# Kernel tuning notes

Measured on AMD Instinct MI355X. Metric: run time of the kernel, lower is better.

Reference implementation:

```python
import jax, jax.numpy as jnp
import numpy as np

KERNEL = 7  # neighborhood window (7x7)
NUM_HEADS = 4


def _window_idx(L, k):
    # NATTEN edge-clamped window start: each query attends to exactly k neighbors.
    starts = jnp.clip(jnp.arange(L) - k // 2, 0, L - k)  # [L]
    return starts[:, None] + jnp.arange(k)[None, :]       # [L, k]


def setup_inputs() -> dict:
    key = jax.random.key(0)
    k1, k2, k3, k4, k5 = jax.random.split(key, 5)
    B, H, W, D = 8, 64, 64, 128
    return {
        "x": jax.random.normal(k1, (B, H, W, D), dtype=jnp.float32),
        "w_qkv": jax.random.normal(k2, (3 * D, D), dtype=jnp.float32) * 0.02,
        "b_qkv": jax.random.normal(k3, (3 * D,), dtype=jnp.float32) * 0.02,
        "w_proj": jax.random.normal(k4, (D, D), dtype=jnp.float32) * 0.02,
        "b_proj": jax.random.normal(k5, (D,), dtype=jnp.float32) * 0.02,
    }


def reference(x, w_qkv, b_qkv, w_proj, b_proj):
    B, H, W, D = x.shape
    nh, k = NUM_HEADS, KERNEL
    hd = D // nh
    scale = hd ** -0.5

    # QKV projection -> [3, B, nh, H, W, hd]
    qkv = x @ w_qkv.T + b_qkv
    qkv = qkv.reshape(B, H, W, 3, nh, hd).transpose(3, 0, 4, 1, 2, 5)
    q, kk, v = qkv[0], qkv[1], qkv[2]

    idx_h = _window_idx(H, k)  # [H, k]
    idx_w = _window_idx(W, k)  # [W, k]
    IH = idx_h[:, None, :, None]  # [H,1,k,1]
    IW = idx_w[None, :, None, :]  # [1,W,1,k]

    # Gather local K/V neighborhoods: [B, nh, H, W, k, k, hd] -> [B, nh, H, W, k*k, hd]
    kn = kk[:, :, IH, IW, :].reshape(B, nh, H, W, k * k, hd)
    vn = v[:, :, IH, IW, :].reshape(B, nh, H, W, k * k, hd)

    attn = jnp.einsum('bhxyd,bhxynd->bhxyn', q * scale, kn)
    attn = jax.nn.softmax(attn, axis=-1)
    out = jnp.einsum('bhxyn,bhxynd->bhxyd', attn, vn)

    out = out.transpose(0, 2, 3, 1, 4).reshape(B, H, W, D)
    return out @ w_proj.T + b_proj
```

## Files before the change

### kernel.cpp

```cpp
#include <hip/hip_runtime.h>
#include <hip/hip_bf16.h>

#define BB 8
#define HH 64
#define WW 64
#define DD 128
#define NH 4
#define HD 32
#define KS 7
#define TS 8
#define HALO 14

typedef __attribute__((ext_vector_type(8))) short short8v;
typedef __attribute__((ext_vector_type(4))) short short4v;
typedef __attribute__((ext_vector_type(4))) float f32x4;
typedef unsigned short bf16_t;

__device__ inline bf16_t f2bf(float f) {
  __hip_bfloat16 h = __float2bfloat16(f);
  return *reinterpret_cast<bf16_t*>(&h);
}

__global__ __launch_bounds__(256) void qkv_mfma(
    const float* __restrict__ x, const float* __restrict__ w,
    const float* __restrict__ bqkv,
    bf16_t* __restrict__ q, bf16_t* __restrict__ k, bf16_t* __restrict__ v) {
  __shared__ __align__(16) short smA[128 * 128];
  __shared__ __align__(16) short smB[128 * 128];
  const int tid = threadIdx.x;
  const int m_tile = blockIdx.x;
  const int n_tile = blockIdx.y;

  const float* Ab = x + (size_t)m_tile * 128 * 128;
  const float* Bb = w + (size_t)n_tile * 128 * 128;
#pragma unroll
  for (int i = 0; i < 8; i++) {
    int idx = tid + i * 256;
    int r = idx >> 4, p = idx & 15;
    const float* ap = Ab + r * 128 + p * 8;
    float4 a0 = *(const float4*)ap;
    float4 a1 = *(const float4*)(ap + 4);
    short8v s;
    s[0] = f2bf(a0.x); s[1] = f2bf(a0.y); s[2] = f2bf(a0.z); s[3] = f2bf(a0.w);
    s[4] = f2bf(a1.x); s[5] = f2bf(a1.y); s[6] = f2bf(a1.z); s[7] = f2bf(a1.w);
    *(short8v*)((char*)smA + ((r * 256 + p * 16) ^ ((r & 7) << 4))) = s;
    const float* bp_ = Bb + r * 128 + p * 8;
    float4 b0 = *(const float4*)bp_;
    float4 b1 = *(const float4*)(bp_ + 4);
    short8v t;
    t[0] = f2bf(b0.x); t[1] = f2bf(b0.y); t[2] = f2bf(b0.z); t[3] = f2bf(b0.w);
    t[4] = f2bf(b1.x); t[5] = f2bf(b1.y); t[6] = f2bf(b1.z); t[7] = f2bf(b1.w);
    *(short8v*)((char*)smB + ((r * 256 + p * 16) ^ ((r & 7) << 4))) = t;
  }
  __syncthreads();

  const int lane = tid & 63;
  const int wid = tid >> 6;
  const int wm = wid >> 1, wn = wid & 1;
  const int l15 = lane & 15, l4 = lane >> 4;

  f32x4 acc[4][4] = {};
  const int rowA0 = wm * 64 + l15;
  const int rowB0 = wn * 64 + l15;
  const int swzA = (rowA0 & 7) << 4;
  const int swzB = (rowB0 & 7) << 4;

#pragma unroll
  for (int ks = 0; ks < 4; ks++) {
    const int cb = ks * 64 + l4 * 16;
    short8v a[4], b[4];
#pragma unroll
    for (int i = 0; i < 4; i++) {
      a[i] = *(const short8v*)((const char*)smA + ((((rowA0 + i * 16) * 256) + cb) ^ swzA));
      b[i] = *(const short8v*)((const char*)smB + ((((rowB0 + i * 16) * 256) + cb) ^ swzB));
    }
#pragma unroll
    for (int mi = 0; mi < 4; mi++)
#pragma unroll
      for (int nj = 0; nj < 4; nj++)
        acc[mi][nj] = __builtin_amdgcn_mfma_f32_16x16x32_bf16(a[mi], b[nj], acc[mi][nj], 0, 0, 0);
  }

  __syncthreads();
  short* smC = smA;
  const float qscale = 0.17677669529663687f;
#pragma unroll
  for (int nj = 0; nj < 4; nj++) {
    const int n_local = wn * 64 + nj * 16 + l15;
    const int n = n_tile * 128 + n_local;
    const float bias = bqkv[n];
    const float sc = (n_tile == 0) ? qscale : 1.f;
#pragma unroll
    for (int mi = 0; mi < 4; mi++) {
#pragma unroll
      for (int r = 0; r < 4; r++) {
        const int m = wm * 64 + mi * 16 + l4 * 4 + r;
        *(bf16_t*)((char*)smC + ((m * 256 + n_local * 2) ^ ((m & 7) << 4))) =
            (bf16_t)f2bf((acc[mi][nj][r] + bias) * sc);
      }
    }
  }
  __syncthreads();

  const int bblk = m_tile >> 5;
  bf16_t* outp = (n_tile == 0) ? q : ((n_tile == 1) ? k : v);
#pragma unroll
  for (int i = 0; i < 8; i++) {
    const int idx = i * 256 + tid;
    const int h = idx >> 9;
    const int rem = idx & 511;
    const int m = rem >> 2, c = rem & 3;
    short8v t8 = *(const short8v*)((const char*)smC +
        ((m * 256 + h * 64 + c * 16) ^ ((m & 7) << 4)));
    const int pix = (m_tile * 128 + m) & 4095;
    *(short8v*)(outp + ((size_t)(bblk * 4 + h)) * 131072 + (size_t)pix * 32 + c * 8) = t8;
  }
}

__global__ __launch_bounds__(256) void attn_mfma(
    const bf16_t* __restrict__ q, const bf16_t* __restrict__ k,
    const bf16_t* __restrict__ v, bf16_t* __restrict__ ao) {
  __shared__ __align__(16) char vtb[16384];

  const int tile = blockIdx.x;
  const int tx = tile >> 3, ty = tile & 7;
  const int head = blockIdx.y, bb = blockIdx.z;
  const size_t bh = ((size_t)bb * NH + head) * 4096;
  const bf16_t* kb = k + bh * HD;
  const bf16_t* vb = v + bh * HD;
  const bf16_t* qb = q + bh * HD;
  const int rstart = min(max(tx * TS - 3, 0), HH - HALO);
  const int cstart = min(max(ty * TS - 3, 0), WW - HALO);
  const int tid = threadIdx.x;
  const int lane = tid & 63, wid = tid >> 6;
  const int l15 = lane & 15, h4 = lane >> 4;

  short8v qf;
  int qx, qy;
  {
    const int pit = wid * 16 + l15;
    qx = tx * TS + (pit >> 3);
    qy = ty * TS + (pit & 7);
    qf = *(const short8v*)(qb + ((size_t)(qx * WW + qy)) * HD + h4 * 8);
  }
  const int wx0 = min(max(qx - 3, 0), HH - KS) - rstart;
  const int wy0 = min(max(qy - 3, 0), WW - KS) - cstart;

  const int x0 = tx * TS + wid * 2;
  const int w0 = min(max(x0 - 3, 0), HH - KS) - rstart;
  const int base = min(w0 & ~1, 4);

  short4v vl[4][2];
#pragma unroll
  for (int t = 0; t < 4; t++) {
    const int idx = tid + t * 256;
    if (idx < 784) {
      const int pp = idx >> 3, c = idx & 7;
      const int pr = pp / 7, pc2 = (pp % 7) * 2;
      const size_t g = ((size_t)((rstart + pr) * WW + (cstart + pc2))) * HD + c * 4;
      vl[t][0] = *(const short4v*)(vb + g);
      vl[t][1] = *(const short4v*)(vb + g + HD);
    }
  }

  f32x4 acc[10];
  const f32x4 zf = {0.f, 0.f, 0.f, 0.f};
  const int kcol = cstart + min(l15, 13);
#pragma unroll
  for (int ch = 0; ch < 2; ch++) {
    short8v kf[5];
#pragma unroll
    for (int i = 0; i < 5; i++) {
      const int pr = rstart + base + ch * 5 + i;
      kf[i] = *(const short8v*)(kb + ((size_t)(pr * WW + kcol)) * HD + h4 * 8);
    }
    __builtin_amdgcn_s_setprio(1);
#pragma unroll
    for (int i = 0; i < 5; i++)
      acc[ch * 5 + i] = __builtin_amdgcn_mfma_f32_16x16x32_bf16(kf[i], qf, zf, 0, 0, 0);
    __builtin_amdgcn_s_setprio(0);
  }

#pragma unroll
  for (int t = 0; t < 4; t++) {
    const int idx = tid + t * 256;
    if (idx < 784) {
      const int pp = idx >> 3, c = idx & 7;
      const int pr = pp / 7, pc2 = (pp % 7) * 2;
      const int pos0 = ((pr >> 1) << 5) + ((pc2 >> 2) << 3) + ((pr & 1) << 2) + (pc2 & 3);
#pragma unroll
      for (int j = 0; j < 4; j++) {
        const int d = c * 4 + j;
        const unsigned pk2 = (unsigned)(unsigned short)vl[t][0][j] |
                             ((unsigned)(unsigned short)vl[t][1][j] << 16);
        *(unsigned*)(vtb + ((d * 512 + pos0 * 2) ^ ((d & 7) << 4))) = pk2;
      }
    }
  }
  for (int idx = tid; idx < 512; idx += 256) {
    const int d = idx >> 4, pr = idx & 15;
    if (pr < 14) {
      const int pos = ((pr >> 1) << 5) + 24 + ((pr & 1) << 2) + 2;
      *(unsigned*)(vtb + ((d * 512 + pos * 2) ^ ((d & 7) << 4))) = 0u;
    }
  }
  __syncthreads();

  bool cv[4];
#pragma unroll
  for (int r = 0; r < 4; r++) cv[r] = ((unsigned)(h4 * 4 + r - wy0) < 7u);
  float sum = 0.f;
#pragma unroll
  for (int nt = 0; nt < 10; nt++) {
    const bool rv = ((unsigned)(base + nt - wx0) < 7u);
#pragma unroll
    for (int r = 0; r < 4; r++) {
      const float p = (rv && cv[r]) ? __expf(acc[nt][r]) : 0.f;
      acc[nt][r] = p;
      sum += p;
    }
  }
  sum += __shfl_xor(sum, 16);
  sum += __shfl_xor(sum, 32);
  const float inv = 1.f / sum;

  f32x4 o0 = zf, o1 = zf;
  const int swzv = (l15 & 7) << 4;
  const int cbase = (base >> 1) * 64;
  __builtin_amdgcn_s_setprio(1);
#pragma unroll
  for (int kc = 0; kc < 5; kc++) {
    union { unsigned u[4]; short8v s; } pa;
    pa.u[0] = (unsigned)f2bf(acc[2 * kc][0] * inv) |
              ((unsigned)f2bf(acc[2 * kc][1] * inv) << 16);
    pa.u[1] = (unsigned)f2bf(acc[2 * kc][2] * inv) |
              ((unsigned)f2bf(acc[2 * kc][3] * inv) << 16);
    pa.u[2] = (unsigned)f2bf(acc[2 * kc + 1][0] * inv) |
              ((unsigned)f2bf(acc[2 * kc + 1][1] * inv) << 16);
    pa.u[3] = (unsigned)f2bf(acc[2 * kc + 1][2] * inv) |
              ((unsigned)f2bf(acc[2 * kc + 1][3] * inv) << 16);
    const int boff = cbase + kc * 64 + h4 * 16;
    short8v vb0 = *(const short8v*)(vtb + ((l15 * 512 + boff) ^ swzv));
    short8v vb1 = *(const short8v*)(vtb + (((l15 + 16) * 512 + boff) ^ swzv));
    o0 = __builtin_amdgcn_mfma_f32_16x16x32_bf16(pa.s, vb0, o0, 0, 0, 0);
    o1 = __builtin_amdgcn_mfma_f32_16x16x32_bf16(pa.s, vb1, o1, 0, 0, 0);
  }
  __builtin_amdgcn_s_setprio(0);

#pragma unroll
  for (int r = 0; r < 4; r++) {
    const int pit = wid * 16 + h4 * 4 + r;
    const int x = tx * TS + (pit >> 3), y = ty * TS + (pit & 7);
    bf16_t* op = ao + ((size_t)bb * 4096 + x * WW + y) * DD + head * HD;
    op[l15]      = (bf16_t)f2bf(o0[r]);
    op[l15 + 16] = (bf16_t)f2bf(o1[r]);
  }
}

__global__ __launch_bounds__(256) void proj_mfma(
    const bf16_t* __restrict__ aob, const float* __restrict__ wp,
    const float* __restrict__ bp, float* __restrict__ out) {
  __shared__ __align__(16) char plds[65536];
  short* smA = (short*)plds;
  short* smB = (short*)(plds + 32768);
  const int tid = threadIdx.x;
  const int m_tile = blockIdx.x;

  const bf16_t* Ab = aob + (size_t)m_tile * 128 * 128;
#pragma unroll
  for (int i = 0; i < 8; i++) {
    int idx = tid + i * 256;
    int r = idx >> 4, p = idx & 15;
    short8v s = *(const short8v*)(Ab + r * 128 + p * 8);
    *(short8v*)((char*)smA + ((r * 256 + p * 16) ^ ((r & 7) << 4))) = s;
    const float* bp_ = wp + r * 128 + p * 8;
    float4 b0 = *(const float4*)bp_;
    float4 b1 = *(const float4*)(bp_ + 4);
    short8v t;
    t[0] = f2bf(b0.x); t[1] = f2bf(b0.y); t[2] = f2bf(b0.z); t[3] = f2bf(b0.w);
    t[4] = f2bf(b1.x); t[5] = f2bf(b1.y); t[6] = f2bf(b1.z); t[7] = f2bf(b1.w);
    *(short8v*)((char*)smB + ((r * 256 + p * 16) ^ ((r & 7) << 4))) = t;
  }
  __syncthreads();

  const int lane = tid & 63;
  const int wid = tid >> 6;
  const int wm = wid >> 1, wn = wid & 1;
  const int l15 = lane & 15, l4 = lane >> 4;

  f32x4 acc[4][4] = {};
  const int rowA0 = wm * 64 + l15;
  const int rowB0 = wn * 64 + l15;
  const int swzA = (rowA0 & 7) << 4;
  const int swzB = (rowB0 & 7) << 4;

#pragma unroll
  for (int ks = 0; ks < 4; ks++) {
    const int cb = ks * 64 + l4 * 16;
    short8v a[4], b[4];
#pragma unroll
    for (int i = 0; i < 4; i++) {
      a[i] = *(const short8v*)((const char*)smA + ((((rowA0 + i * 16) * 256) + cb) ^ swzA));
      b[i] = *(const short8v*)((const char*)smB + ((((rowB0 + i * 16) * 256) + cb) ^ swzB));
    }
#pragma unroll
    for (int mi = 0; mi < 4; mi++)
#pragma unroll
      for (int nj = 0; nj < 4; nj++)
        acc[mi][nj] = __builtin_amdgcn_mfma_f32_16x16x32_bf16(a[mi], b[nj], acc[mi][nj], 0, 0, 0);
  }

  __syncthreads();
#pragma unroll
  for (int nj = 0; nj < 4; nj++) {
    const int n = wn * 64 + nj * 16 + l15;
    const float bias = bp[n];
#pragma unroll
    for (int mi = 0; mi < 4; mi++) {
#pragma unroll
      for (int r = 0; r < 4; r++) {
        const int m = wm * 64 + mi * 16 + l4 * 4 + r;
        *(float*)(plds + ((m * 512 + n * 4) ^ ((m & 7) << 5))) = acc[mi][nj][r] + bias;
      }
    }
  }
  __syncthreads();

#pragma unroll
  for (int i = 0; i < 16; i++) {
    const int idx = i * 256 + tid;
    const int m = idx >> 5, c = idx & 31;
    float4 t = *(const float4*)(plds + ((m * 512 + c * 16) ^ ((m & 7) << 5)));
    *(float4*)(out + (size_t)(m_tile * 128 + m) * DD + c * 4) = t;
  }
}

extern "C" void kernel_launch(void* const* d_in, const int* in_sizes, int n_in,
                              void* d_out, int out_size, void* d_ws, size_t ws_size,
                              hipStream_t stream) {
  const float* x      = (const float*)d_in[0];
  const float* w_qkv  = (const float*)d_in[1];
  const float* b_qkv  = (const float*)d_in[2];
  const float* w_proj = (const float*)d_in[3];
  const float* b_proj = (const float*)d_in[4];
  float* out = (float*)d_out;

  const size_t per = (size_t)BB * NH * HH * WW * HD;
  bf16_t* q  = (bf16_t*)d_ws;
  bf16_t* k  = q + per;
  bf16_t* v  = k + per;
  bf16_t* ao = v + per;

  qkv_mfma<<<dim3(256, 3), dim3(256), 0, stream>>>(x, w_qkv, b_qkv, q, k, v);
  attn_mfma<<<dim3(64, NH, BB), dim3(256), 0, stream>>>(q, k, v, ao);
  proj_mfma<<<dim3(256), dim3(256), 0, stream>>>(ao, w_proj, b_proj, out);
}
```

Measured before the change: 43.74 us.

## Pre-convert weights to bf16 and shrink GEMM tiles, reading B from global

Adds a small kernel that converts the QKV and projection weights to bf16 once per call, so the GEMM kernels no longer convert fp32 weights per block. The QKV GEMM tile shrinks from 128 to 64 rows and the projection tile from 128 to 32 rows, which raises the block count and cuts LDS use. Weight fragments are now loaded straight from global memory instead of being staged in LDS. In exchange there is an extra kernel launch and more redundant weight reads across blocks, served from cache.

```diff
diff --git a/kernel.cpp b/kernel.cpp
--- a/kernel.cpp
+++ b/kernel.cpp
@@ -21,20 +21,34 @@
   return *reinterpret_cast<bf16_t*>(&h);
 }
 
+__global__ __launch_bounds__(256) void convert_w(
+    const float* __restrict__ wq, const float* __restrict__ wp,
+    bf16_t* __restrict__ wqb, bf16_t* __restrict__ wpb) {
+  const int chunk = blockIdx.x * 256 + threadIdx.x;
+  if (chunk < 12288) {
+    float4 t = *(const float4*)(wq + chunk * 4);
+    short4v s = {(short)f2bf(t.x), (short)f2bf(t.y), (short)f2bf(t.z), (short)f2bf(t.w)};
+    *(short4v*)(wqb + chunk * 4) = s;
+  } else {
+    const int c2 = chunk - 12288;
+    float4 t = *(const float4*)(wp + c2 * 4);
+    short4v s = {(short)f2bf(t.x), (short)f2bf(t.y), (short)f2bf(t.z), (short)f2bf(t.w)};
+    *(short4v*)(wpb + c2 * 4) = s;
+  }
+}
+
 __global__ __launch_bounds__(256) void qkv_mfma(
-    const float* __restrict__ x, const float* __restrict__ w,
+    const float* __restrict__ x, const bf16_t* __restrict__ wqb,
     const float* __restrict__ bqkv,
     bf16_t* __restrict__ q, bf16_t* __restrict__ k, bf16_t* __restrict__ v) {
-  __shared__ __align__(16) short smA[128 * 128];
-  __shared__ __align__(16) short smB[128 * 128];
+  __shared__ __align__(16) short smA[64 * 128];
   const int tid = threadIdx.x;
   const int m_tile = blockIdx.x;
   const int n_tile = blockIdx.y;
 
-  const float* Ab = x + (size_t)m_tile * 128 * 128;
-  const float* Bb = w + (size_t)n_tile * 128 * 128;
-#pragma unroll
-  for (int i = 0; i < 8; i++) {
+  const float* Ab = x + (size_t)m_tile * 64 * 128;
+#pragma unroll
+  for (int i = 0; i < 4; i++) {
     int idx = tid + i * 256;
     int r = idx >> 4, p = idx & 15;
     const float* ap = Ab + r * 128 + p * 8;
@@ -44,38 +58,34 @@
     s[0] = f2bf(a0.x); s[1] = f2bf(a0.y); s[2] = f2bf(a0.z); s[3] = f2bf(a0.w);
     s[4] = f2bf(a1.x); s[5] = f2bf(a1.y); s[6] = f2bf(a1.z); s[7] = f2bf(a1.w);
     *(short8v*)((char*)smA + ((r * 256 + p * 16) ^ ((r & 7) << 4))) = s;
-    const float* bp_ = Bb + r * 128 + p * 8;
-    float4 b0 = *(const float4*)bp_;
-    float4 b1 = *(const float4*)(bp_ + 4);
-    short8v t;
-    t[0] = f2bf(b0.x); t[1] = f2bf(b0.y); t[2] = f2bf(b0.z); t[3] = f2bf(b0.w);
-    t[4] = f2bf(b1.x); t[5] = f2bf(b1.y); t[6] = f2bf(b1.z); t[7] = f2bf(b1.w);
-    *(short8v*)((char*)smB + ((r * 256 + p * 16) ^ ((r & 7) << 4))) = t;
-  }
-  __syncthreads();
-
-  const int lane = tid & 63;
-  const int wid = tid >> 6;
+  }
+  __syncthreads();
+
+  const int lane = tid & 63, wid = tid >> 6;
   const int wm = wid >> 1, wn = wid & 1;
   const int l15 = lane & 15, l4 = lane >> 4;
 
-  f32x4 acc[4][4] = {};
-  const int rowA0 = wm * 64 + l15;
-  const int rowB0 = wn * 64 + l15;
+  f32x4 acc[2][4] = {};
+  const int rowA0 = wm * 32 + l15;
   const int swzA = (rowA0 & 7) << 4;
-  const int swzB = (rowB0 & 7) << 4;
+  const bf16_t* wb = wqb + (size_t)(n_tile * 128) * 128;
 
 #pragma unroll
   for (int ks = 0; ks < 4; ks++) {
     const int cb = ks * 64 + l4 * 16;
-    short8v a[4], b[4];
-#pragma unroll
-    for (int i = 0; i < 4; i++) {
-      a[i] = *(const short8v*)((const char*)smA + ((((rowA0 + i * 16) * 256) + cb) ^ swzA));
-      b[i] = *(const short8v*)((const char*)smB + ((((rowB0 + i * 16) * 256) + cb) ^ swzB));
-    }
-#pragma unroll
-    for (int mi = 0; mi < 4; mi++)
+    const int k0 = ks * 32 + l4 * 8;
+    short8v a[2], b[4];
+#pragma unroll
+    for (int mi = 0; mi < 2; mi++)
+      a[mi] = *(const short8v*)((const char*)smA +
+                ((((rowA0 + mi * 16) * 256) + cb) ^ swzA));
+#pragma unroll
+    for (int nj = 0; nj < 4; nj++) {
+      const int rowB = wn * 64 + nj * 16 + l15;
+      b[nj] = *(const short8v*)(wb + (size_t)rowB * 128 + k0);
+    }
+#pragma unroll
+    for (int mi = 0; mi < 2; mi++)
 #pragma unroll
       for (int nj = 0; nj < 4; nj++)
         acc[mi][nj] = __builtin_amdgcn_mfma_f32_16x16x32_bf16(a[mi], b[nj], acc[mi][nj], 0, 0, 0);
@@ -84,35 +94,34 @@
   __syncthreads();
   short* smC = smA;
   const float qscale = 0.17677669529663687f;
+  const float sc = (n_tile == 0) ? qscale : 1.f;
 #pragma unroll
   for (int nj = 0; nj < 4; nj++) {
     const int n_local = wn * 64 + nj * 16 + l15;
-    const int n = n_tile * 128 + n_local;
-    const float bias = bqkv[n];
-    const float sc = (n_tile == 0) ? qscale : 1.f;
-#pragma unroll
-    for (int mi = 0; mi < 4; mi++) {
+    const float bias = bqkv[n_tile * 128 + n_local];
+#pragma unroll
+    for (int mi = 0; mi < 2; mi++) {
 #pragma unroll
       for (int r = 0; r < 4; r++) {
-        const int m = wm * 64 + mi * 16 + l4 * 4 + r;
+        const int m = wm * 32 + mi * 16 + l4 * 4 + r;
         *(bf16_t*)((char*)smC + ((m * 256 + n_local * 2) ^ ((m & 7) << 4))) =
-            (bf16_t)f2bf((acc[mi][nj][r] + bias) * sc);
+            f2bf((acc[mi][nj][r] + bias) * sc);
       }
     }
   }
   __syncthreads();
 
-  const int bblk = m_tile >> 5;
+  const int bblk = m_tile >> 6;
   bf16_t* outp = (n_tile == 0) ? q : ((n_tile == 1) ? k : v);
 #pragma unroll
-  for (int i = 0; i < 8; i++) {
+  for (int i = 0; i < 4; i++) {
     const int idx = i * 256 + tid;
-    const int h = idx >> 9;
-    const int rem = idx & 511;
+    const int h = idx >> 8;
+    const int rem = idx & 255;
     const int m = rem >> 2, c = rem & 3;
     short8v t8 = *(const short8v*)((const char*)smC +
         ((m * 256 + h * 64 + c * 16) ^ ((m & 7) << 4)));
-    const int pix = (m_tile * 128 + m) & 4095;
+    const int pix = (m_tile * 64 + m) & 4095;
     *(short8v*)(outp + ((size_t)(bblk * 4 + h)) * 131072 + (size_t)pix * 32 + c * 8) = t8;
   }
 }
@@ -258,56 +267,45 @@
 }
 
 __global__ __launch_bounds__(256) void proj_mfma(
-    const bf16_t* __restrict__ aob, const float* __restrict__ wp,
+    const bf16_t* __restrict__ aob, const bf16_t* __restrict__ wpb,
     const float* __restrict__ bp, float* __restrict__ out) {
-  __shared__ __align__(16) char plds[65536];
+  __shared__ __align__(16) char plds[16384];
   short* smA = (short*)plds;
-  short* smB = (short*)(plds + 32768);
   const int tid = threadIdx.x;
   const int m_tile = blockIdx.x;
 
-  const bf16_t* Ab = aob + (size_t)m_tile * 128 * 128;
-#pragma unroll
-  for (int i = 0; i < 8; i++) {
+  const bf16_t* Ab = aob + (size_t)m_tile * 32 * 128;
+#pragma unroll
+  for (int i = 0; i < 2; i++) {
     int idx = tid + i * 256;
     int r = idx >> 4, p = idx & 15;
     short8v s = *(const short8v*)(Ab + r * 128 + p * 8);
     *(short8v*)((char*)smA + ((r * 256 + p * 16) ^ ((r & 7) << 4))) = s;
-    const float* bp_ = wp + r * 128 + p * 8;
-    float4 b0 = *(const float4*)bp_;
-    float4 b1 = *(const float4*)(bp_ + 4);
-    short8v t;
-    t[0] = f2bf(b0.x); t[1] = f2bf(b0.y); t[2] = f2bf(b0.z); t[3] = f2bf(b0.w);
-    t[4] = f2bf(b1.x); t[5] = f2bf(b1.y); t[6] = f2bf(b1.z); t[7] = f2bf(b1.w);
-    *(short8v*)((char*)smB + ((r * 256 + p * 16) ^ ((r & 7) << 4))) = t;
-  }
-  __syncthreads();
-
-  const int lane = tid & 63;
-  const int wid = tid >> 6;
+  }
+  __syncthreads();
+
+  const int lane = tid & 63, wid = tid >> 6;
   const int wm = wid >> 1, wn = wid & 1;
   const int l15 = lane & 15, l4 = lane >> 4;
 
-  f32x4 acc[4][4] = {};
-  const int rowA0 = wm * 64 + l15;
-  const int rowB0 = wn * 64 + l15;
+  f32x4 acc[4] = {};
+  const int rowA0 = wm * 16 + l15;
   const int swzA = (rowA0 & 7) << 4;
-  const int swzB = (rowB0 & 7) << 4;
 
 #pragma unroll
   for (int ks = 0; ks < 4; ks++) {
     const int cb = ks * 64 + l4 * 16;
-    short8v a[4], b[4];
-#pragma unroll
-    for (int i = 0; i < 4; i++) {
-      a[i] = *(const short8v*)((const char*)smA + ((((rowA0 + i * 16) * 256) + cb) ^ swzA));
-      b[i] = *(const short8v*)((const char*)smB + ((((rowB0 + i * 16) * 256) + cb) ^ swzB));
-    }
-#pragma unroll
-    for (int mi = 0; mi < 4; mi++)
-#pragma unroll
-      for (int nj = 0; nj < 4; nj++)
-        acc[mi][nj] = __builtin_amdgcn_mfma_f32_16x16x32_bf16(a[mi], b[nj], acc[mi][nj], 0, 0, 0);
+    const int k0 = ks * 32 + l4 * 8;
+    short8v a = *(const short8v*)((const char*)smA + (((rowA0 * 256) + cb) ^ swzA));
+    short8v b[4];
+#pragma unroll
+    for (int nj = 0; nj < 4; nj++) {
+      const int rowB = wn * 64 + nj * 16 + l15;
+      b[nj] = *(const short8v*)(wpb + (size_t)rowB * 128 + k0);
+    }
+#pragma unroll
+    for (int nj = 0; nj < 4; nj++)
+      acc[nj] = __builtin_amdgcn_mfma_f32_16x16x32_bf16(a, b[nj], acc[nj], 0, 0, 0);
   }
 
   __syncthreads();
@@ -316,22 +314,19 @@
     const int n = wn * 64 + nj * 16 + l15;
     const float bias = bp[n];
 #pragma unroll
-    for (int mi = 0; mi < 4; mi++) {
-#pragma unroll
-      for (int r = 0; r < 4; r++) {
-        const int m = wm * 64 + mi * 16 + l4 * 4 + r;
-        *(float*)(plds + ((m * 512 + n * 4) ^ ((m & 7) << 5))) = acc[mi][nj][r] + bias;
-      }
-    }
-  }
-  __syncthreads();
-
-#pragma unroll
-  for (int i = 0; i < 16; i++) {
+    for (int r = 0; r < 4; r++) {
+      const int m = wm * 16 + l4 * 4 + r;
+      *(float*)(plds + ((m * 512 + n * 4) ^ ((m & 7) << 5))) = acc[nj][r] + bias;
+    }
+  }
+  __syncthreads();
+
+#pragma unroll
+  for (int i = 0; i < 4; i++) {
     const int idx = i * 256 + tid;
     const int m = idx >> 5, c = idx & 31;
     float4 t = *(const float4*)(plds + ((m * 512 + c * 16) ^ ((m & 7) << 5)));
-    *(float4*)(out + (size_t)(m_tile * 128 + m) * DD + c * 4) = t;
+    *(float4*)(out + (size_t)(m_tile * 32 + m) * DD + c * 4) = t;
   }
 }
 
@@ -346,12 +341,15 @@
   float* out = (float*)d_out;
 
   const size_t per = (size_t)BB * NH * HH * WW * HD;
-  bf16_t* q  = (bf16_t*)d_ws;
-  bf16_t* k  = q + per;
-  bf16_t* v  = k + per;
-  bf16_t* ao = v + per;
-
-  qkv_mfma<<<dim3(256, 3), dim3(256), 0, stream>>>(x, w_qkv, b_qkv, q, k, v);
+  bf16_t* q   = (bf16_t*)d_ws;
+  bf16_t* k   = q + per;
+  bf16_t* v   = k + per;
+  bf16_t* ao  = v + per;
+  bf16_t* wqb = ao + per;
+  bf16_t* wpb = wqb + 49152;
+
+  convert_w<<<dim3(64), dim3(256), 0, stream>>>(w_qkv, w_proj, wqb, wpb);
+  qkv_mfma<<<dim3(512, 3), dim3(256), 0, stream>>>(x, wqb, b_qkv, q, k, v);
   attn_mfma<<<dim3(64, NH, BB), dim3(256), 0, stream>>>(q, k, v, ao);
-  proj_mfma<<<dim3(256), dim3(256), 0, stream>>>(ao, w_proj, b_proj, out);
-}
+  proj_mfma<<<dim3(1024), dim3(256), 0, stream>>>(ao, wpb, b_proj, out);
+}
```

Measured after the change: 59.35 us. 1.36x slower.
